# Kernel tuning notes

Measured on AMD Instinct MI355X. Metric: run time of the kernel, lower is better.

## Reference

```python
import jax, jax.numpy as jnp
import numpy as np

N_NODES = 20000
N_EDGES = 160000
IN_DIM = 512
HID = 256
N_CLASSES = 2
NUM_GRAPHS = 16


def setup_inputs() -> dict:
    key = jax.random.key(0)
    ks = jax.random.split(key, 12)
    x = jax.random.normal(ks[0], (N_NODES, IN_DIM), dtype=jnp.float32)
    edge_index = jax.random.randint(ks[1], (2, N_EDGES), 0, N_NODES, dtype=jnp.int64)
    batch = jnp.sort(jax.random.randint(ks[2], (N_NODES,), 0, NUM_GRAPHS, dtype=jnp.int64))
    def glorot(k, shape):
        lim = float(np.sqrt(6.0 / (shape[0] + shape[1])))
        return jax.random.uniform(k, shape, jnp.float32, -lim, lim)
    return {
        "x": x,
        "edge_index": edge_index,
        "batch": batch,
        "W1n": glorot(ks[3], (IN_DIM, HID)),
        "W1s": glorot(ks[4], (IN_DIM, HID)),
        "b1": jnp.zeros((HID,), jnp.float32),
        "W2n": glorot(ks[5], (HID, HID)),
        "W2s": glorot(ks[6], (HID, HID)),
        "b2": jnp.zeros((HID,), jnp.float32),
        "fc1w": glorot(ks[7], (HID, HID // 2)),
        "fc1b": jnp.zeros((HID // 2,), jnp.float32),
        "fc2w": glorot(ks[8], (HID // 2, N_CLASSES)),
        "fc2b": jnp.zeros((N_CLASSES,), jnp.float32),
    }


def _sage_conv(x, W_nbr, W_self, b, src, dst, n_nodes):
    # mean-aggregate neighbor features (messages flow src -> dst, PyG convention)
    deg = jax.ops.segment_sum(jnp.ones(src.shape, x.dtype), dst, num_segments=n_nodes)
    deg = jnp.maximum(deg, 1.0)
    aggr = jax.ops.segment_sum(x[src], dst, num_segments=n_nodes) / deg[:, None]
    # SAGEConv: lin_l(aggr) + lin_r(x) + bias (equivalent to concat-linear)
    return aggr @ W_nbr + x @ W_self + b


def reference(x, edge_index, batch, W1n, W1s, b1, W2n, W2s, b2, fc1w, fc1b, fc2w, fc2b):
    src, dst = edge_index[0], edge_index[1]
    n = x.shape[0]
    h = jax.nn.relu(_sage_conv(x, W1n, W1s, b1, src, dst, n))
    h = jax.nn.relu(_sage_conv(h, W2n, W2s, b2, src, dst, n))
    # global_mean_pool over graph ids
    cnt = jax.ops.segment_sum(jnp.ones((n,), h.dtype), batch, num_segments=NUM_GRAPHS)
    pooled = jax.ops.segment_sum(h, batch, num_segments=NUM_GRAPHS) / jnp.maximum(cnt, 1.0)[:, None]
    out = jax.nn.relu(pooled @ fc1w + fc1b) @ fc2w + fc2b
    return out
```

## Files before the change

kernel.cpp:

```cpp
#include <hip/hip_runtime.h>
#include <hip/hip_bf16.h>


#define HID 256
#define NCOL 512

typedef __bf16 bf16x8 __attribute__((ext_vector_type(8)));
typedef float floatx4 __attribute__((ext_vector_type(4)));
typedef unsigned int u32;
typedef const u32 __attribute__((address_space(1)))* gp_t;
typedef u32 __attribute__((address_space(3)))* lp_t;

__device__ __forceinline__ ushort f2bf(float f) {
    unsigned u = __float_as_uint(f);
    u += 0x7fffu + ((u >> 16) & 1u);
    return (ushort)(u >> 16);
}
__device__ __forceinline__ float bf2f(ushort b) {
    return __uint_as_float(((unsigned)b) << 16);
}

__device__ __forceinline__ void packT_work(const float* __restrict__ Wn,
                                           const float* __restrict__ Ws,
                                           ushort* __restrict__ WT, int K, int gid) {
    if (gid >= NCOL * K) return;
    int n = gid / K, k = gid - n * K;
    float v = (n < HID) ? Wn[k * HID + n] : Ws[k * HID + (n - HID)];
    WT[gid] = f2bf(v);
}

__global__ void prep_kernel(const float* __restrict__ x, ushort* __restrict__ xb, int n4,
                            const float* __restrict__ W1n, const float* __restrict__ W1s,
                            ushort* __restrict__ w1t, int K1,
                            const float* __restrict__ W2n, const float* __restrict__ W2s,
                            ushort* __restrict__ w2t, int K2,
                            const int* __restrict__ dst, int* __restrict__ degi, int n_edges,
                            int nb_cvt, int nb_w1, int nb_w2) {
    int bx = blockIdx.x, t = threadIdx.x;
    if (bx < nb_cvt) {
        int i = bx * 256 + t;
        if (i < n4) {
            float4 v = ((const float4*)x)[i];
            ushort4 o;
            o.x = f2bf(v.x); o.y = f2bf(v.y); o.z = f2bf(v.z); o.w = f2bf(v.w);
            ((ushort4*)xb)[i] = o;
        }
    } else if (bx < nb_cvt + nb_w1) {
        packT_work(W1n, W1s, w1t, K1, (bx - nb_cvt) * 256 + t);
    } else if (bx < nb_cvt + nb_w1 + nb_w2) {
        packT_work(W2n, W2s, w2t, K2, (bx - nb_cvt - nb_w1) * 256 + t);
    } else {
        int e = (bx - nb_cvt - nb_w1 - nb_w2) * 256 + t;
        if (e < n_edges) atomicAdd(&degi[dst[e]], 1);
    }
}

__global__ __launch_bounds__(256) void psum_kernel(const int* __restrict__ degi,
                                                   int* __restrict__ partials, int n) {
    int t = threadIdx.x;
    int i = blockIdx.x * 256 + t;
    int v = (i < n) ? degi[i] : 0;
#pragma unroll
    for (int d = 1; d < 64; d <<= 1) v += __shfl_xor(v, d, 64);
    __shared__ int wsum[4];
    if ((t & 63) == 0) wsum[t >> 6] = v;
    __syncthreads();
    if (t == 0) partials[blockIdx.x] = wsum[0] + wsum[1] + wsum[2] + wsum[3];
}

__global__ __launch_bounds__(64) void pscan_kernel(int* __restrict__ partials,
                                                   int* __restrict__ off, int nb, int n) {
    int lane = threadIdx.x;
    int carry = 0;
    for (int base = 0; base < nb; base += 256) {
        int i0 = base + lane * 4;
        int v0 = (i0 + 0 < nb) ? partials[i0 + 0] : 0;
        int v1 = (i0 + 1 < nb) ? partials[i0 + 1] : 0;
        int v2 = (i0 + 2 < nb) ? partials[i0 + 2] : 0;
        int v3 = (i0 + 3 < nb) ? partials[i0 + 3] : 0;
        int local = v0 + v1 + v2 + v3;
        int s = local;
#pragma unroll
        for (int d = 1; d < 64; d <<= 1) {
            int t = __shfl_up(s, d, 64);
            if (lane >= d) s += t;
        }
        int excl = carry + s - local;
        if (i0 + 0 < nb) partials[i0 + 0] = excl;
        excl += v0;
        if (i0 + 1 < nb) partials[i0 + 1] = excl;
        excl += v1;
        if (i0 + 2 < nb) partials[i0 + 2] = excl;
        excl += v2;
        if (i0 + 3 < nb) partials[i0 + 3] = excl;
        carry += __shfl(s, 63, 64);
    }
    if (lane == 0) off[n] = carry;
}

__global__ __launch_bounds__(256) void scan2_kernel(const int* __restrict__ degi,
                                                    const int* __restrict__ partials,
                                                    int* __restrict__ off,
                                                    int* __restrict__ cursor, int n) {
    int t = threadIdx.x, lane = t & 63, w = t >> 6;
    int i = blockIdx.x * 256 + t;
    int v = (i < n) ? degi[i] : 0;
    int s = v;
#pragma unroll
    for (int d = 1; d < 64; d <<= 1) {
        int u = __shfl_up(s, d, 64);
        if (lane >= d) s += u;
    }
    __shared__ int wsum[4];
    if (lane == 63) wsum[w] = s;
    __syncthreads();
    int woff = 0;
    for (int k = 0; k < w; ++k) woff += wsum[k];
    int excl = partials[blockIdx.x] + woff + s - v;
    if (i < n) { off[i] = excl; cursor[i] = excl; }
}

__global__ void fill_kernel(const int* __restrict__ src, const int* __restrict__ dst,
                            int* __restrict__ cursor, int* __restrict__ eidx, int n_edges) {
    int e = blockIdx.x * 256 + threadIdx.x;
    if (e < n_edges) {
        int p = atomicAdd(&cursor[dst[e]], 1);
        eidx[p] = src[e];
    }
}

__global__ __launch_bounds__(256) void gemm_mfma(const ushort* __restrict__ A,
                                                 const ushort* __restrict__ BT,
                                                 ushort* __restrict__ Y, int K) {
    __shared__ ushort As[2][64 * 64];
    __shared__ ushort Bs[2][128 * 64];
    int tid = threadIdx.x;
    int w = tid >> 6, lane = tid & 63;
    int quad = lane >> 4, r16 = lane & 15;
    int m0 = blockIdx.y * 64, n0 = blockIdx.x * 128;
    int wm = (w >> 1) * 32, wn = (w & 1) * 64;

    int arow[2], agu[2], brow[4], bgu[4];
#pragma unroll
    for (int rr = 0; rr < 2; ++rr) {
        int idx = rr * 256 + tid;
        arow[rr] = idx >> 3;
        agu[rr] = (idx & 7) ^ (arow[rr] & 7);
    }
#pragma unroll
    for (int rr = 0; rr < 4; ++rr) {
        int idx = rr * 256 + tid;
        brow[rr] = idx >> 3;
        bgu[rr] = (idx & 7) ^ (brow[rr] & 7);
    }

    auto stage = [&](int buf, int k0) {
#pragma unroll
        for (int rr = 0; rr < 2; ++rr) {
            const ushort* ga = A + (size_t)(m0 + arow[rr]) * K + k0 + agu[rr] * 8;
            ushort* la = As[buf] + (size_t)(rr * 256 + w * 64) * 8;
            __builtin_amdgcn_global_load_lds((gp_t)(const void*)ga, (lp_t)(void*)la, 16, 0, 0);
        }
#pragma unroll
        for (int rr = 0; rr < 4; ++rr) {
            const ushort* gb = BT + (size_t)(n0 + brow[rr]) * K + k0 + bgu[rr] * 8;
            ushort* lb = Bs[buf] + (size_t)(rr * 256 + w * 64) * 8;
            __builtin_amdgcn_global_load_lds((gp_t)(const void*)gb, (lp_t)(void*)lb, 16, 0, 0);
        }
    };

    floatx4 acc[2][4];
#pragma unroll
    for (int i = 0; i < 2; ++i)
#pragma unroll
        for (int j = 0; j < 4; ++j) acc[i][j] = (floatx4){0.f, 0.f, 0.f, 0.f};

    const int nk = K >> 6;
    stage(0, 0);
    for (int t = 0; t < nk; ++t) {
        int cb = t & 1;
        __syncthreads();
        if (t + 1 < nk) stage(cb ^ 1, (t + 1) << 6);
        const ushort* Ab = As[cb];
        const ushort* Bb = Bs[cb];
#pragma unroll
        for (int s = 0; s < 2; ++s) {
            bf16x8 a[2], b[4];
#pragma unroll
            for (int i = 0; i < 2; ++i) {
                int row = wm + i * 16 + r16;
                int au = (s * 4 + quad) ^ (row & 7);
                a[i] = *(const bf16x8*)(Ab + row * 64 + au * 8);
            }
#pragma unroll
            for (int j = 0; j < 4; ++j) {
                int row = wn + j * 16 + r16;
                int bu = (s * 4 + quad) ^ (row & 7);
                b[j] = *(const bf16x8*)(Bb + row * 64 + bu * 8);
            }
#pragma unroll
            for (int i = 0; i < 2; ++i)
#pragma unroll
                for (int j = 0; j < 4; ++j)
                    acc[i][j] = __builtin_amdgcn_mfma_f32_16x16x32_bf16(a[i], b[j], acc[i][j], 0, 0, 0);
        }
    }
#pragma unroll
    for (int i = 0; i < 2; ++i)
#pragma unroll
        for (int j = 0; j < 4; ++j) {
            int col = n0 + wn + j * 16 + r16;
#pragma unroll
            for (int rg = 0; rg < 4; ++rg) {
                int row = m0 + wm + i * 16 + quad * 4 + rg;
                Y[(size_t)row * NCOL + col] = f2bf(acc[i][j][rg]);
            }
        }
}

__global__ __launch_bounds__(256) void gather_kernel(const ushort* __restrict__ Y,
                                                     const int* __restrict__ off,
                                                     const int* __restrict__ eidx,
                                                     const float* __restrict__ bias,
                                                     ushort* __restrict__ h, int n_nodes) {
    int tid = threadIdx.x;
    int v = blockIdx.x * 4 + (tid >> 6);
    if (v >= n_nodes) return;
    int q4 = (tid & 63) << 2;
    int e0 = off[v], e1 = off[v + 1];
    ushort4 sv = *(const ushort4*)(Y + (size_t)v * NCOL + HID + q4);
    float4 b = *(const float4*)(bias + q4);
    float4 a0 = make_float4(0.f, 0.f, 0.f, 0.f), a1 = a0, a2 = a0, a3 = a0;
    int e = e0;
    for (; e + 3 < e1; e += 4) {
        int s0 = eidx[e], s1 = eidx[e + 1], s2 = eidx[e + 2], s3 = eidx[e + 3];
        ushort4 y0 = *(const ushort4*)(Y + (size_t)s0 * NCOL + q4);
        ushort4 y1 = *(const ushort4*)(Y + (size_t)s1 * NCOL + q4);
        ushort4 y2 = *(const ushort4*)(Y + (size_t)s2 * NCOL + q4);
        ushort4 y3 = *(const ushort4*)(Y + (size_t)s3 * NCOL + q4);
        a0.x += bf2f(y0.x); a0.y += bf2f(y0.y); a0.z += bf2f(y0.z); a0.w += bf2f(y0.w);
        a1.x += bf2f(y1.x); a1.y += bf2f(y1.y); a1.z += bf2f(y1.z); a1.w += bf2f(y1.w);
        a2.x += bf2f(y2.x); a2.y += bf2f(y2.y); a2.z += bf2f(y2.z); a2.w += bf2f(y2.w);
        a3.x += bf2f(y3.x); a3.y += bf2f(y3.y); a3.z += bf2f(y3.z); a3.w += bf2f(y3.w);
    }
    for (; e < e1; ++e) {
        ushort4 y = *(const ushort4*)(Y + (size_t)eidx[e] * NCOL + q4);
        a0.x += bf2f(y.x); a0.y += bf2f(y.y); a0.z += bf2f(y.z); a0.w += bf2f(y.w);
    }
    float invd = 1.0f / fmaxf((float)(e1 - e0), 1.0f);
    ushort4 r;
    r.x = f2bf(fmaxf((a0.x + a1.x + a2.x + a3.x) * invd + bf2f(sv.x) + b.x, 0.f));
    r.y = f2bf(fmaxf((a0.y + a1.y + a2.y + a3.y) * invd + bf2f(sv.y) + b.y, 0.f));
    r.z = f2bf(fmaxf((a0.z + a1.z + a2.z + a3.z) * invd + bf2f(sv.z) + b.z, 0.f));
    r.w = f2bf(fmaxf((a0.w + a1.w + a2.w + a3.w) * invd + bf2f(sv.w) + b.w, 0.f));
    *(ushort4*)(h + (size_t)v * HID + q4) = r;
}

__global__ void pool_kernel(const ushort* __restrict__ h, const int* __restrict__ batch,
                            float* __restrict__ pooled, float* __restrict__ cnt, int n_nodes) {
    int f = threadIdx.x;
    int v0 = blockIdx.x * 64;
    int vend = min(v0 + 64, n_nodes);
    if (v0 >= n_nodes) return;
    int cur = batch[v0];
    float acc = 0.f, ac = 0.f;
    for (int v = v0; v < vend; ++v) {
        int g = batch[v];
        if (g != cur) {
            atomicAdd(&pooled[cur * HID + f], acc);
            if (f == 0) atomicAdd(&cnt[cur], ac);
            acc = 0.f; ac = 0.f; cur = g;
        }
        acc += bf2f(h[(size_t)v * HID + f]);
        ac += 1.0f;
    }
    atomicAdd(&pooled[cur * HID + f], acc);
    if (f == 0) atomicAdd(&cnt[cur], ac);
}

__global__ void head_kernel(const float* __restrict__ pooled, const float* __restrict__ cnt,
                            const float* __restrict__ fc1w, const float* __restrict__ fc1b,
                            const float* __restrict__ fc2w, const float* __restrict__ fc2b,
                            float* __restrict__ out) {
    int g = blockIdx.x, j = threadIdx.x;
    __shared__ float p[256];
    __shared__ float hid[128];
    float inv = 1.0f / fmaxf(cnt[g], 1.0f);
    p[j] = pooled[g * HID + j] * inv;
    p[j + 128] = pooled[g * HID + 128 + j] * inv;
    __syncthreads();
    float a = fc1b[j];
    for (int f = 0; f < 256; ++f) a += p[f] * fc1w[f * 128 + j];
    hid[j] = fmaxf(a, 0.f);
    __syncthreads();
    if (j < 2) {
        float o = fc2b[j];
        for (int t = 0; t < 128; ++t) o += hid[t] * fc2w[t * 2 + j];
        out[g * 2 + j] = o;
    }
}

extern "C" void kernel_launch(void* const* d_in, const int* in_sizes, int n_in,
                              void* d_out, int out_size, void* d_ws, size_t ws_size,
                              hipStream_t stream) {
    const float* x    = (const float*)d_in[0];
    const int*   ei   = (const int*)d_in[1];
    const int*   batch= (const int*)d_in[2];
    const float* W1n  = (const float*)d_in[3];
    const float* W1s  = (const float*)d_in[4];
    const float* b1   = (const float*)d_in[5];
    const float* W2n  = (const float*)d_in[6];
    const float* W2s  = (const float*)d_in[7];
    const float* b2   = (const float*)d_in[8];
    const float* fc1w = (const float*)d_in[9];
    const float* fc1b = (const float*)d_in[10];
    const float* fc2w = (const float*)d_in[11];
    const float* fc2b = (const float*)d_in[12];
    float* out = (float*)d_out;

    const int n_nodes = in_sizes[2];
    const int n_edges = in_sizes[1] / 2;
    const int in_dim  = in_sizes[0] / n_nodes;
    const int Mpad    = (n_nodes + 63) & ~63;
    const int nb      = (n_nodes + 255) / 256;
    const int* src = ei;
    const int* dst = ei + n_edges;

    char* wsb = (char*)d_ws;
    size_t cur = 0;
    auto alloc = [&](size_t nbytes) { size_t o = cur; cur = (cur + nbytes + 255) & ~(size_t)255; return o; };
    size_t o_degi = alloc((size_t)n_nodes * 4);
    size_t o_off  = alloc((size_t)(n_nodes + 1) * 4);
    size_t o_cur  = alloc((size_t)n_nodes * 4);
    size_t o_part = alloc((size_t)nb * 4);
    size_t o_eidx = alloc((size_t)n_edges * 4);
    size_t o_w1   = alloc((size_t)NCOL * in_dim * 2);
    size_t o_w2   = alloc((size_t)NCOL * HID * 2);
    size_t o_xb   = alloc((size_t)Mpad * in_dim * 2);
    size_t o_hb   = alloc((size_t)Mpad * HID * 2);
    size_t o_y    = alloc((size_t)Mpad * NCOL * 2);
    size_t o_pool = alloc((size_t)16 * HID * 4 + 16 * 4);
    (void)ws_size;

    int*    degi    = (int*)(wsb + o_degi);
    int*    off     = (int*)(wsb + o_off);
    int*    cursor  = (int*)(wsb + o_cur);
    int*    partials= (int*)(wsb + o_part);
    int*    eidx    = (int*)(wsb + o_eidx);
    ushort* w1t     = (ushort*)(wsb + o_w1);
    ushort* w2t     = (ushort*)(wsb + o_w2);
    ushort* xb      = (ushort*)(wsb + o_xb);
    ushort* hb      = (ushort*)(wsb + o_hb);
    ushort* Y       = (ushort*)(wsb + o_y);
    float*  pooled  = (float*)(wsb + o_pool);
    float*  cnt     = pooled + 16 * HID;

    hipMemsetAsync(degi, 0, (size_t)n_nodes * 4, stream);
    hipMemsetAsync(pooled, 0, (size_t)(16 * HID + 16) * 4, stream);

    int n4 = n_nodes * in_dim / 4;
    int nb_cvt = (n4 + 255) / 256;
    int nb_w1  = (NCOL * in_dim + 255) / 256;
    int nb_w2  = (NCOL * HID + 255) / 256;
    int nb_deg = (n_edges + 255) / 256;
    prep_kernel<<<nb_cvt + nb_w1 + nb_w2 + nb_deg, 256, 0, stream>>>(
        x, xb, n4, W1n, W1s, w1t, in_dim, W2n, W2s, w2t, HID,
        dst, degi, n_edges, nb_cvt, nb_w1, nb_w2);

    psum_kernel<<<nb, 256, 0, stream>>>(degi, partials, n_nodes);
    pscan_kernel<<<1, 64, 0, stream>>>(partials, off, nb, n_nodes);
    scan2_kernel<<<nb, 256, 0, stream>>>(degi, partials, off, cursor, n_nodes);
    fill_kernel<<<(n_edges + 255) / 256, 256, 0, stream>>>(src, dst, cursor, eidx, n_edges);

    dim3 gemm_grid(NCOL / 128, Mpad / 64);
    int gather_blocks = (n_nodes + 3) / 4;

    gemm_mfma<<<gemm_grid, 256, 0, stream>>>(xb, w1t, Y, in_dim);
    gather_kernel<<<gather_blocks, 256, 0, stream>>>(Y, off, eidx, b1, hb, n_nodes);

    gemm_mfma<<<gemm_grid, 256, 0, stream>>>(hb, w2t, Y, HID);
    gather_kernel<<<gather_blocks, 256, 0, stream>>>(Y, off, eidx, b2, hb, n_nodes);

    pool_kernel<<<(n_nodes + 63) / 64, 256, 0, stream>>>(hb, batch, pooled, cnt, n_nodes);
    head_kernel<<<16, 128, 0, stream>>>(pooled, cnt, fc1w, fc1b, fc2w, fc2b, out);
}
```

Before: 231.6 us.

## Fuse mean-pool into second gather and remap GEMM blocks by XCD

The separate pool kernel is removed. The second-layer gather now atomically adds each node's fp32 post-ReLU row into its graph's pooled accumulator, so the layer-2 hidden state is never written to or read back from memory. The GEMM launch becomes a 1D grid whose block ids are remapped so the four column tiles of one row tile land on the same XCD, aiming for better L2 reuse of A. In exchange, the fused pooling issues one float atomic per node feature onto only 16×256 addresses, which risks heavy atomic contention and makes the summation order nondeterministic.

```diff
diff --git a/kernel.cpp b/kernel.cpp
--- a/kernel.cpp
+++ b/kernel.cpp
@@ -131,13 +131,19 @@
 
 __global__ __launch_bounds__(256) void gemm_mfma(const ushort* __restrict__ A,
                                                  const ushort* __restrict__ BT,
-                                                 ushort* __restrict__ Y, int K) {
+                                                 ushort* __restrict__ Y, int K, int nG) {
+    int b = blockIdx.x;
+    int xcd = b & 7, rest = b >> 3;
+    int m = rest & 3, Ggrp = rest >> 2;
+    int G = xcd + 8 * Ggrp;
+    if (G >= nG) return;
+    int m0 = G * 64, n0 = m * 128;
+
     __shared__ ushort As[2][64 * 64];
     __shared__ ushort Bs[2][128 * 64];
     int tid = threadIdx.x;
     int w = tid >> 6, lane = tid & 63;
     int quad = lane >> 4, r16 = lane & 15;
-    int m0 = blockIdx.y * 64, n0 = blockIdx.x * 128;
     int wm = (w >> 1) * 32, wn = (w & 1) * 64;
 
     int arow[2], agu[2], brow[4], bgu[4];
@@ -185,7 +191,7 @@
         const ushort* Bb = Bs[cb];
 #pragma unroll
         for (int s = 0; s < 2; ++s) {
-            bf16x8 a[2], b[4];
+            bf16x8 a[2], b2[4];
 #pragma unroll
             for (int i = 0; i < 2; ++i) {
                 int row = wm + i * 16 + r16;
@@ -196,13 +202,13 @@
             for (int j = 0; j < 4; ++j) {
                 int row = wn + j * 16 + r16;
                 int bu = (s * 4 + quad) ^ (row & 7);
-                b[j] = *(const bf16x8*)(Bb + row * 64 + bu * 8);
+                b2[j] = *(const bf16x8*)(Bb + row * 64 + bu * 8);
             }
 #pragma unroll
             for (int i = 0; i < 2; ++i)
 #pragma unroll
                 for (int j = 0; j < 4; ++j)
-                    acc[i][j] = __builtin_amdgcn_mfma_f32_16x16x32_bf16(a[i], b[j], acc[i][j], 0, 0, 0);
+                    acc[i][j] = __builtin_amdgcn_mfma_f32_16x16x32_bf16(a[i], b2[j], acc[i][j], 0, 0, 0);
         }
     }
 #pragma unroll
@@ -218,15 +224,11 @@
         }
 }
 
-__global__ __launch_bounds__(256) void gather_kernel(const ushort* __restrict__ Y,
-                                                     const int* __restrict__ off,
-                                                     const int* __restrict__ eidx,
-                                                     const float* __restrict__ bias,
-                                                     ushort* __restrict__ h, int n_nodes) {
-    int tid = threadIdx.x;
-    int v = blockIdx.x * 4 + (tid >> 6);
-    if (v >= n_nodes) return;
-    int q4 = (tid & 63) << 2;
+__device__ __forceinline__ float4 gather_row(const ushort* __restrict__ Y,
+                                             const int* __restrict__ off,
+                                             const int* __restrict__ eidx,
+                                             const float* __restrict__ bias,
+                                             int v, int q4) {
     int e0 = off[v], e1 = off[v + 1];
     ushort4 sv = *(const ushort4*)(Y + (size_t)v * NCOL + HID + q4);
     float4 b = *(const float4*)(bias + q4);
@@ -248,34 +250,46 @@
         a0.x += bf2f(y.x); a0.y += bf2f(y.y); a0.z += bf2f(y.z); a0.w += bf2f(y.w);
     }
     float invd = 1.0f / fmaxf((float)(e1 - e0), 1.0f);
-    ushort4 r;
-    r.x = f2bf(fmaxf((a0.x + a1.x + a2.x + a3.x) * invd + bf2f(sv.x) + b.x, 0.f));
-    r.y = f2bf(fmaxf((a0.y + a1.y + a2.y + a3.y) * invd + bf2f(sv.y) + b.y, 0.f));
-    r.z = f2bf(fmaxf((a0.z + a1.z + a2.z + a3.z) * invd + bf2f(sv.z) + b.z, 0.f));
-    r.w = f2bf(fmaxf((a0.w + a1.w + a2.w + a3.w) * invd + bf2f(sv.w) + b.w, 0.f));
-    *(ushort4*)(h + (size_t)v * HID + q4) = r;
-}
-
-__global__ void pool_kernel(const ushort* __restrict__ h, const int* __restrict__ batch,
-                            float* __restrict__ pooled, float* __restrict__ cnt, int n_nodes) {
-    int f = threadIdx.x;
-    int v0 = blockIdx.x * 64;
-    int vend = min(v0 + 64, n_nodes);
-    if (v0 >= n_nodes) return;
-    int cur = batch[v0];
-    float acc = 0.f, ac = 0.f;
-    for (int v = v0; v < vend; ++v) {
-        int g = batch[v];
-        if (g != cur) {
-            atomicAdd(&pooled[cur * HID + f], acc);
-            if (f == 0) atomicAdd(&cnt[cur], ac);
-            acc = 0.f; ac = 0.f; cur = g;
-        }
-        acc += bf2f(h[(size_t)v * HID + f]);
-        ac += 1.0f;
-    }
-    atomicAdd(&pooled[cur * HID + f], acc);
-    if (f == 0) atomicAdd(&cnt[cur], ac);
+    float4 r;
+    r.x = fmaxf((a0.x + a1.x + a2.x + a3.x) * invd + bf2f(sv.x) + b.x, 0.f);
+    r.y = fmaxf((a0.y + a1.y + a2.y + a3.y) * invd + bf2f(sv.y) + b.y, 0.f);
+    r.z = fmaxf((a0.z + a1.z + a2.z + a3.z) * invd + bf2f(sv.z) + b.z, 0.f);
+    r.w = fmaxf((a0.w + a1.w + a2.w + a3.w) * invd + bf2f(sv.w) + b.w, 0.f);
+    return r;
+}
+
+__global__ __launch_bounds__(256) void gather_kernel(const ushort* __restrict__ Y,
+                                                     const int* __restrict__ off,
+                                                     const int* __restrict__ eidx,
+                                                     const float* __restrict__ bias,
+                                                     ushort* __restrict__ h, int n_nodes) {
+    int tid = threadIdx.x;
+    int v = blockIdx.x * 4 + (tid >> 6);
+    if (v >= n_nodes) return;
+    int q4 = (tid & 63) << 2;
+    float4 r = gather_row(Y, off, eidx, bias, v, q4);
+    ushort4 o;
+    o.x = f2bf(r.x); o.y = f2bf(r.y); o.z = f2bf(r.z); o.w = f2bf(r.w);
+    *(ushort4*)(h + (size_t)v * HID + q4) = o;
+}
+
+__global__ __launch_bounds__(256) void gather_pool_kernel(const ushort* __restrict__ Y,
+                                                          const int* __restrict__ off,
+                                                          const int* __restrict__ eidx,
+                                                          const float* __restrict__ bias,
+                                                          const int* __restrict__ batch,
+                                                          float* __restrict__ pooled,
+                                                          float* __restrict__ cnt, int n_nodes) {
+    int tid = threadIdx.x;
+    int v = blockIdx.x * 4 + (tid >> 6);
+    if (v >= n_nodes) return;
+    int q4 = (tid & 63) << 2;
+    float4 r = gather_row(Y, off, eidx, bias, v, q4);
+    int g = batch[v];
+    float* p = pooled + g * HID + q4;
+    atomicAdd(p + 0, r.x); atomicAdd(p + 1, r.y);
+    atomicAdd(p + 2, r.z); atomicAdd(p + 3, r.w);
+    if ((tid & 63) == 0) atomicAdd(&cnt[g], 1.0f);
 }
 
 __global__ void head_kernel(const float* __restrict__ pooled, const float* __restrict__ cnt,
@@ -323,6 +337,7 @@
     const int in_dim  = in_sizes[0] / n_nodes;
     const int Mpad    = (n_nodes + 63) & ~63;
     const int nb      = (n_nodes + 255) / 256;
+    const int nG      = Mpad / 64;
     const int* src = ei;
     const int* dst = ei + n_edges;
 
@@ -372,15 +387,15 @@
     scan2_kernel<<<nb, 256, 0, stream>>>(degi, partials, off, cursor, n_nodes);
     fill_kernel<<<(n_edges + 255) / 256, 256, 0, stream>>>(src, dst, cursor, eidx, n_edges);
 
-    dim3 gemm_grid(NCOL / 128, Mpad / 64);
+    int gemm_blocks = 8 * 4 * ((nG + 7) / 8);
     int gather_blocks = (n_nodes + 3) / 4;
 
-    gemm_mfma<<<gemm_grid, 256, 0, stream>>>(xb, w1t, Y, in_dim);
+    gemm_mfma<<<gemm_blocks, 256, 0, stream>>>(xb, w1t, Y, in_dim, nG);
     gather_kernel<<<gather_blocks, 256, 0, stream>>>(Y, off, eidx, b1, hb, n_nodes);
 
-    gemm_mfma<<<gemm_grid, 256, 0, stream>>>(hb, w2t, Y, HID);
-    gather_kernel<<<gather_blocks, 256, 0, stream>>>(Y, off, eidx, b2, hb, n_nodes);
-
-    pool_kernel<<<(n_nodes + 63) / 64, 256, 0, stream>>>(hb, batch, pooled, cnt, n_nodes);
+    gemm_mfma<<<gemm_blocks, 256, 0, stream>>>(hb, w2t, Y, HID, nG);
+    gather_pool_kernel<<<gather_blocks, 256, 0, stream>>>(Y, off, eidx, b2, batch,
+                                                          pooled, cnt, n_nodes);
+
     head_kernel<<<16, 128, 0, stream>>>(pooled, cnt, fc1w, fc1b, fc2w, fc2b, out);
 }
```

After: 530.3 us. 129% more time.
